# Kernel tuning notes

Measured on AMD Instinct MI355X. Metric: run time of the kernel, lower is better.

Reference implementation:

```python
import jax, jax.numpy as jnp
import numpy as np

SCALE = 8.0  # sqrt(d_k), d_k = 64

def setup_inputs() -> dict:
    key = jax.random.key(0)
    kq, kk, kv = jax.random.split(key, 3)
    B, S, D = 32, 2048, 64
    q = jax.random.normal(kq, (B, S, D), dtype=jnp.float32)
    k = jax.random.normal(kk, (B, S, D), dtype=jnp.float32)
    v = jax.random.normal(kv, (B, S, D), dtype=jnp.float32)
    return {"q": q, "k": k, "v": v}

def reference(q, k, v):
    # scores: [B, Sq, Skv]
    scores = jnp.einsum('bqd,bkd->bqk', q, k) / SCALE
    attn = jax.nn.softmax(scores, axis=2)
    # out: [B, Sq, D]
    return jnp.einsum('bqk,bkd->bqd', attn, v)
```

## Files before the change

### kernel.cpp

```cpp
#include <hip/hip_runtime.h>

#define S_N 2048
#define D_H 64
#define KVB 64
#define NT (S_N / KVB)

typedef _Float16 half8 __attribute__((ext_vector_type(8)));
typedef float floatx4 __attribute__((ext_vector_type(4)));
typedef float floatx16 __attribute__((ext_vector_type(16)));
typedef unsigned int uint2v __attribute__((ext_vector_type(2)));

__device__ __forceinline__ unsigned pkh(float a, float b) {
  return __builtin_bit_cast(unsigned, __builtin_amdgcn_cvt_pkrtz(a, b));
}
__device__ __forceinline__ float bcf(unsigned u) { return __builtin_bit_cast(float, u); }
__device__ __forceinline__ unsigned bcu(float f) { return __builtin_bit_cast(unsigned, f); }

__device__ __forceinline__ int sig(int r) { return ((r & 7) + ((r >> 3) & 7)) & 7; }

__global__ __launch_bounds__(256, 2) void sdpa_kernel(
    const float* __restrict__ Q, const float* __restrict__ K,
    const float* __restrict__ V, float* __restrict__ O) {
  const int tid = threadIdx.x;
  const int wv = tid >> 6;
  const int l = tid & 63;
  const int c31 = l & 31;
  const int hi = l >> 5;

  __shared__ _Float16 KS[2][KVB * D_H];
  __shared__ _Float16 VS[2][D_H * KVB];

  const size_t bbase = (size_t)blockIdx.y * S_N * D_H;
  const int qbase = blockIdx.x * 128 + wv * 32;
  const int qrow = qbase + c31;

  const float SCL = 0.125f * 1.44269504088896f;

  half8 qf[4];
#pragma unroll
  for (int kc = 0; kc < 4; ++kc) {
    const float* qp = Q + bbase + (size_t)qrow * D_H + kc * 16 + hi * 8;
    floatx4 x = *(const floatx4*)qp;
    floatx4 y = *(const floatx4*)(qp + 4);
    union { unsigned u[4]; half8 h; } uu = {{
        pkh(x[0] * SCL, x[1] * SCL), pkh(x[2] * SCL, x[3] * SCL),
        pkh(y[0] * SCL, y[1] * SCL), pkh(y[2] * SCL, y[3] * SCL)}};
    qf[kc] = uu.h;
  }

  const int kr_ = tid >> 3;
  const int kg8 = tid & 7;

  floatx4 kreg[2][2], vreg[2][2];

  auto loadKV = [&](int kv0) {
#pragma unroll
    for (int it = 0; it < 2; ++it) {
      const float* kp = K + bbase + (size_t)(kv0 + it * 32 + kr_) * D_H + kg8 * 8;
      kreg[it][0] = *(const floatx4*)kp;
      kreg[it][1] = *(const floatx4*)(kp + 4);
    }
#pragma unroll
    for (int r = 0; r < 2; ++r) {
      const float* vp = V + bbase + (size_t)(kv0 + 2 * kr_ + r) * D_H + kg8 * 8;
      vreg[r][0] = *(const floatx4*)vp;
      vreg[r][1] = *(const floatx4*)(vp + 4);
    }
  };

  auto writeKV = [&](int buf) {
#pragma unroll
    for (int it = 0; it < 2; ++it) {
      int row = it * 32 + kr_;
      int g = kg8 ^ sig(row);
      union { unsigned u[4]; half8 h; } uu = {{
          pkh(kreg[it][0][0], kreg[it][0][1]), pkh(kreg[it][0][2], kreg[it][0][3]),
          pkh(kreg[it][1][0], kreg[it][1][1]), pkh(kreg[it][1][2], kreg[it][1][3])}};
      *(half8*)(&KS[buf][row * 64 + g * 8]) = uu.h;
    }
#pragma unroll
    for (int jj = 0; jj < 8; ++jj) {
      int d = kg8 * 8 + jj;
      int g = (kr_ >> 2) ^ ((jj + kg8) & 7);
      unsigned val = pkh(vreg[0][jj >> 2][jj & 3], vreg[1][jj >> 2][jj & 3]);
      *(unsigned*)((char*)&VS[buf][0] + d * 128 + g * 16 + (kr_ & 3) * 4) = val;
    }
  };

  floatx16 oo[2] = {{0,0,0,0,0,0,0,0,0,0,0,0,0,0,0,0},
                    {0,0,0,0,0,0,0,0,0,0,0,0,0,0,0,0}};
  float m_ = -__builtin_inff();
  float l_ = 0.0f;

  loadKV(0);
  writeKV(0);
  __syncthreads();

  for (int t = 0; t < NT; ++t) {
    const int cur = t & 1;
    const bool pf = (t + 1) < NT;
    if (pf) loadKV((t + 1) * KVB);

    floatx16 st0 = {0,0,0,0,0,0,0,0,0,0,0,0,0,0,0,0};
    floatx16 st1 = {0,0,0,0,0,0,0,0,0,0,0,0,0,0,0,0};
    {
      const int sg0 = sig(c31), sg1 = sig(32 + c31);
#pragma unroll
      for (int kc = 0; kc < 4; ++kc) {
        half8 kf0 = *(const half8*)(&KS[cur][c31 * 64 + (((2 * kc + hi) ^ sg0) * 8)]);
        st0 = __builtin_amdgcn_mfma_f32_32x32x16_f16(kf0, qf[kc], st0, 0, 0, 0);
        half8 kf1 = *(const half8*)(&KS[cur][(32 + c31) * 64 + (((2 * kc + hi) ^ sg1) * 8)]);
        st1 = __builtin_amdgcn_mfma_f32_32x32x16_f16(kf1, qf[kc], st1, 0, 0, 0);
      }
    }

    float tm = st0[0];
#pragma unroll
    for (int r = 1; r < 16; ++r) tm = fmaxf(tm, st0[r]);
#pragma unroll
    for (int r = 0; r < 16; ++r) tm = fmaxf(tm, st1[r]);
    {
      uint2v rr = __builtin_amdgcn_permlane32_swap(bcu(tm), bcu(tm), false, false);
      tm = fmaxf(bcf(rr[0]), bcf(rr[1]));
    }
    bool skip = __all(tm <= m_ + 8.0f);
    float mn = skip ? m_ : fmaxf(m_, tm);
    float alpha = skip ? 1.0f : __builtin_amdgcn_exp2f(m_ - mn);
    m_ = mn;
    float ps = 0.0f;
#pragma unroll
    for (int r = 0; r < 16; ++r) { float p = __builtin_amdgcn_exp2f(st0[r] - mn); st0[r] = p; ps += p; }
#pragma unroll
    for (int r = 0; r < 16; ++r) { float p = __builtin_amdgcn_exp2f(st1[r] - mn); st1[r] = p; ps += p; }
    {
      uint2v rr = __builtin_amdgcn_permlane32_swap(bcu(ps), bcu(ps), false, false);
      ps = bcf(rr[0]) + bcf(rr[1]);
    }
    if (!skip) {
      l_ *= alpha;
#pragma unroll
      for (int r = 0; r < 16; ++r) { oo[0][r] *= alpha; oo[1][r] *= alpha; }
    }
    l_ += ps;

    unsigned wds[16];
#pragma unroll
    for (int j = 0; j < 8; ++j) wds[j] = pkh(st0[2 * j], st0[2 * j + 1]);
#pragma unroll
    for (int j = 0; j < 8; ++j) wds[8 + j] = pkh(st1[2 * j], st1[2 * j + 1]);
    half8 pfrag[4];
#pragma unroll
    for (int kcc = 0; kcc < 4; ++kcc) {
      int base = (kcc >> 1) * 8 + 4 * (kcc & 1);
      uint2v r0 = __builtin_amdgcn_permlane32_swap(wds[base + 0], wds[base + 2], false, false);
      uint2v r1 = __builtin_amdgcn_permlane32_swap(wds[base + 1], wds[base + 3], false, false);
      union { unsigned u[4]; half8 h; } uu = {{r0[0], r1[0], r0[1], r1[1]}};
      pfrag[kcc] = uu.h;
    }

    if (pf) writeKV(cur ^ 1);

#pragma unroll
    for (int dsub = 0; dsub < 2; ++dsub) {
      const int row = dsub * 32 + c31;
      const int sg = sig(row);
#pragma unroll
      for (int kcc = 0; kcc < 4; ++kcc) {
        half8 vf = *(const half8*)(&VS[cur][row * 64 + (((2 * kcc + hi) ^ sg) * 8)]);
        oo[dsub] = __builtin_amdgcn_mfma_f32_32x32x16_f16(vf, pfrag[kcc], oo[dsub], 0, 0, 0);
      }
    }

    __syncthreads();
  }

  float inv = 1.0f / l_;
  float* op = O + bbase + (size_t)qrow * D_H;
#pragma unroll
  for (int dsub = 0; dsub < 2; ++dsub) {
#pragma unroll
    for (int u = 0; u < 4; ++u) {
      floatx4 w;
#pragma unroll
      for (int i = 0; i < 4; ++i) w[i] = oo[dsub][4 * u + i] * inv;
      *(floatx4*)(op + dsub * 32 + u * 8 + hi * 4) = w;
    }
  }
}

extern "C" void kernel_launch(void* const* d_in, const int* in_sizes, int n_in,
                              void* d_out, int out_size, void* d_ws, size_t ws_size,
                              hipStream_t stream) {
  const float* q = (const float*)d_in[0];
  const float* k = (const float*)d_in[1];
  const float* v = (const float*)d_in[2];
  float* o = (float*)d_out;
  dim3 grid(S_N / 128, 32);
  sdpa_kernel<<<grid, dim3(256), 0, stream>>>(q, k, v, o);
}
```

Measured before the change: 145.8 us.

## Use 64-query blocks of two waves, XCD-aware block remap, tree reductions

Shrinks each workgroup from four waves (128 query rows) to two waves (64 rows), doubling the grid to 1024 blocks, and remaps the linear block id so that consecutive blocks of the same batch land on the same XCD for L2 reuse of K/V. The K/V staging loops are widened so 128 threads still fill the 64x64 tiles. Row max and sum reductions are rebalanced into trees to shorten the dependency chains. The trade-off is that each block loads K/V for fewer queries, which doubles total global K/V traffic, and with two blocks per CU there may be fewer resident waves.

```diff
diff --git a/kernel.cpp b/kernel.cpp
--- a/kernel.cpp
+++ b/kernel.cpp
@@ -4,6 +4,8 @@
 #define D_H 64
 #define KVB 64
 #define NT (S_N / KVB)
+#define QBLK 64
+#define NBLK (32 * (S_N / QBLK))
 
 typedef _Float16 half8 __attribute__((ext_vector_type(8)));
 typedef float floatx4 __attribute__((ext_vector_type(4)));
@@ -18,7 +20,7 @@
 
 __device__ __forceinline__ int sig(int r) { return ((r & 7) + ((r >> 3) & 7)) & 7; }
 
-__global__ __launch_bounds__(256, 2) void sdpa_kernel(
+__global__ __launch_bounds__(128, 2) void sdpa_kernel(
     const float* __restrict__ Q, const float* __restrict__ K,
     const float* __restrict__ V, float* __restrict__ O) {
   const int tid = threadIdx.x;
@@ -30,9 +32,13 @@
   __shared__ _Float16 KS[2][KVB * D_H];
   __shared__ _Float16 VS[2][D_H * KVB];
 
-  const size_t bbase = (size_t)blockIdx.y * S_N * D_H;
-  const int qbase = blockIdx.x * 128 + wv * 32;
-  const int qrow = qbase + c31;
+  const int bid = blockIdx.x;
+  const int nid = (bid & 7) * (NBLK / 8) + (bid >> 3);
+  const int b = nid >> 5;
+  const int qt = nid & 31;
+
+  const size_t bbase = (size_t)b * S_N * D_H;
+  const int qrow = qt * QBLK + wv * 32 + c31;
 
   const float SCL = 0.125f * 1.44269504088896f;
 
@@ -48,42 +54,51 @@
     qf[kc] = uu.h;
   }
 
-  const int kr_ = tid >> 3;
-  const int kg8 = tid & 7;
-
-  floatx4 kreg[2][2], vreg[2][2];
+  const int r8 = tid >> 3;
+  const int g8 = tid & 7;
+
+  floatx4 kreg[4][2];
+  floatx4 vreg[2][2][2];
 
   auto loadKV = [&](int kv0) {
 #pragma unroll
-    for (int it = 0; it < 2; ++it) {
-      const float* kp = K + bbase + (size_t)(kv0 + it * 32 + kr_) * D_H + kg8 * 8;
+    for (int it = 0; it < 4; ++it) {
+      const float* kp = K + bbase + (size_t)(kv0 + it * 16 + r8) * D_H + g8 * 8;
       kreg[it][0] = *(const floatx4*)kp;
       kreg[it][1] = *(const floatx4*)(kp + 4);
     }
 #pragma unroll
-    for (int r = 0; r < 2; ++r) {
-      const float* vp = V + bbase + (size_t)(kv0 + 2 * kr_ + r) * D_H + kg8 * 8;
-      vreg[r][0] = *(const floatx4*)vp;
-      vreg[r][1] = *(const floatx4*)(vp + 4);
+    for (int rr = 0; rr < 2; ++rr) {
+      int kvp = rr * 16 + r8;
+#pragma unroll
+      for (int r = 0; r < 2; ++r) {
+        const float* vp = V + bbase + (size_t)(kv0 + 2 * kvp + r) * D_H + g8 * 8;
+        vreg[rr][r][0] = *(const floatx4*)vp;
+        vreg[rr][r][1] = *(const floatx4*)(vp + 4);
+      }
     }
   };
 
   auto writeKV = [&](int buf) {
 #pragma unroll
-    for (int it = 0; it < 2; ++it) {
-      int row = it * 32 + kr_;
-      int g = kg8 ^ sig(row);
+    for (int it = 0; it < 4; ++it) {
+      int row = it * 16 + r8;
+      int g = g8 ^ sig(row);
       union { unsigned u[4]; half8 h; } uu = {{
           pkh(kreg[it][0][0], kreg[it][0][1]), pkh(kreg[it][0][2], kreg[it][0][3]),
           pkh(kreg[it][1][0], kreg[it][1][1]), pkh(kreg[it][1][2], kreg[it][1][3])}};
       *(half8*)(&KS[buf][row * 64 + g * 8]) = uu.h;
     }
 #pragma unroll
-    for (int jj = 0; jj < 8; ++jj) {
-      int d = kg8 * 8 + jj;
-      int g = (kr_ >> 2) ^ ((jj + kg8) & 7);
-      unsigned val = pkh(vreg[0][jj >> 2][jj & 3], vreg[1][jj >> 2][jj & 3]);
-      *(unsigned*)((char*)&VS[buf][0] + d * 128 + g * 16 + (kr_ & 3) * 4) = val;
+    for (int rr = 0; rr < 2; ++rr) {
+      int kvp = rr * 16 + r8;
+#pragma unroll
+      for (int jj = 0; jj < 8; ++jj) {
+        int d = g8 * 8 + jj;
+        int g = (kvp >> 2) ^ ((jj + g8) & 7);
+        unsigned val = pkh(vreg[rr][0][jj >> 2][jj & 3], vreg[rr][1][jj >> 2][jj & 3]);
+        *(unsigned*)((char*)&VS[buf][0] + d * 128 + g * 16 + (kvp & 3) * 4) = val;
+      }
     }
   };
 
@@ -114,11 +129,13 @@
       }
     }
 
-    float tm = st0[0];
-#pragma unroll
-    for (int r = 1; r < 16; ++r) tm = fmaxf(tm, st0[r]);
-#pragma unroll
-    for (int r = 0; r < 16; ++r) tm = fmaxf(tm, st1[r]);
+    float mx[8];
+#pragma unroll
+    for (int j = 0; j < 8; ++j)
+      mx[j] = fmaxf(fmaxf(st0[j], st0[j + 8]), fmaxf(st1[j], st1[j + 8]));
+    float m01 = fmaxf(mx[0], mx[1]), m23 = fmaxf(mx[2], mx[3]);
+    float m45 = fmaxf(mx[4], mx[5]), m67 = fmaxf(mx[6], mx[7]);
+    float tm = fmaxf(fmaxf(m01, m23), fmaxf(m45, m67));
     {
       uint2v rr = __builtin_amdgcn_permlane32_swap(bcu(tm), bcu(tm), false, false);
       tm = fmaxf(bcf(rr[0]), bcf(rr[1]));
@@ -127,11 +144,17 @@
     float mn = skip ? m_ : fmaxf(m_, tm);
     float alpha = skip ? 1.0f : __builtin_amdgcn_exp2f(m_ - mn);
     m_ = mn;
-    float ps = 0.0f;
-#pragma unroll
-    for (int r = 0; r < 16; ++r) { float p = __builtin_amdgcn_exp2f(st0[r] - mn); st0[r] = p; ps += p; }
-#pragma unroll
-    for (int r = 0; r < 16; ++r) { float p = __builtin_amdgcn_exp2f(st1[r] - mn); st1[r] = p; ps += p; }
+#pragma unroll
+    for (int r = 0; r < 16; ++r) st0[r] = __builtin_amdgcn_exp2f(st0[r] - mn);
+#pragma unroll
+    for (int r = 0; r < 16; ++r) st1[r] = __builtin_amdgcn_exp2f(st1[r] - mn);
+    float sp[8];
+#pragma unroll
+    for (int j = 0; j < 8; ++j)
+      sp[j] = (st0[j] + st0[j + 8]) + (st1[j] + st1[j + 8]);
+    float s01 = sp[0] + sp[1], s23 = sp[2] + sp[3];
+    float s45 = sp[4] + sp[5], s67 = sp[6] + sp[7];
+    float ps = (s01 + s23) + (s45 + s67);
     {
       uint2v rr = __builtin_amdgcn_permlane32_swap(bcu(ps), bcu(ps), false, false);
       ps = bcf(rr[0]) + bcf(rr[1]);
@@ -195,6 +218,5 @@
   const float* k = (const float*)d_in[1];
   const float* v = (const float*)d_in[2];
   float* o = (float*)d_out;
-  dim3 grid(S_N / 128, 32);
-  sdpa_kernel<<<grid, dim3(256), 0, stream>>>(q, k, v, o);
+  sdpa_kernel<<<dim3(NBLK), dim3(128), 0, stream>>>(q, k, v, o);
 }
```

New measurement: 166.9 us. +14.4%, slower.

## Quad-buffer K/V in LDS, move barrier, add MFMA priority and XCD block swizzle

Applied to the files above, without the earlier changes.

Expands the K/V LDS ring from 2 to 4 buffers so the single barrier can sit between the prefetch write and the PV MFMAs instead of at the end of each iteration. Raises wave priority around the MFMA sections and reorders the max and sum reductions into trees to shorten dependency chains. Switches to a 1D grid with a block-id swizzle that groups blocks of the same batch onto the same XCD for better L2 reuse. LDS use doubles to 64KB per block, which may limit occupancy to two blocks per CU.

```diff
diff --git a/kernel.cpp b/kernel.cpp
--- a/kernel.cpp
+++ b/kernel.cpp
@@ -4,6 +4,8 @@
 #define D_H 64
 #define KVB 64
 #define NT (S_N / KVB)
+#define QBLK 128
+#define NBLK (32 * (S_N / QBLK))
 
 typedef _Float16 half8 __attribute__((ext_vector_type(8)));
 typedef float floatx4 __attribute__((ext_vector_type(4)));
@@ -27,12 +29,16 @@
   const int c31 = l & 31;
   const int hi = l >> 5;
 
-  __shared__ _Float16 KS[2][KVB * D_H];
-  __shared__ _Float16 VS[2][D_H * KVB];
-
-  const size_t bbase = (size_t)blockIdx.y * S_N * D_H;
-  const int qbase = blockIdx.x * 128 + wv * 32;
-  const int qrow = qbase + c31;
+  __shared__ _Float16 KS[4][KVB * D_H];
+  __shared__ _Float16 VS[4][D_H * KVB];
+
+  const int bid = blockIdx.x;
+  const int nid = (bid & 7) * (NBLK / 8) + (bid >> 3);
+  const int b = nid >> 4;
+  const int qt = nid & 15;
+
+  const size_t bbase = (size_t)b * S_N * D_H;
+  const int qrow = qt * QBLK + wv * 32 + c31;
 
   const float SCL = 0.125f * 1.44269504088896f;
 
@@ -97,7 +103,7 @@
   __syncthreads();
 
   for (int t = 0; t < NT; ++t) {
-    const int cur = t & 1;
+    const int cur = t & 3;
     const bool pf = (t + 1) < NT;
     if (pf) loadKV((t + 1) * KVB);
 
@@ -105,6 +111,7 @@
     floatx16 st1 = {0,0,0,0,0,0,0,0,0,0,0,0,0,0,0,0};
     {
       const int sg0 = sig(c31), sg1 = sig(32 + c31);
+      __builtin_amdgcn_s_setprio(1);
 #pragma unroll
       for (int kc = 0; kc < 4; ++kc) {
         half8 kf0 = *(const half8*)(&KS[cur][c31 * 64 + (((2 * kc + hi) ^ sg0) * 8)]);
@@ -112,13 +119,16 @@
         half8 kf1 = *(const half8*)(&KS[cur][(32 + c31) * 64 + (((2 * kc + hi) ^ sg1) * 8)]);
         st1 = __builtin_amdgcn_mfma_f32_32x32x16_f16(kf1, qf[kc], st1, 0, 0, 0);
       }
-    }
-
-    float tm = st0[0];
-#pragma unroll
-    for (int r = 1; r < 16; ++r) tm = fmaxf(tm, st0[r]);
-#pragma unroll
-    for (int r = 0; r < 16; ++r) tm = fmaxf(tm, st1[r]);
+      __builtin_amdgcn_s_setprio(0);
+    }
+
+    float mx[8];
+#pragma unroll
+    for (int j = 0; j < 8; ++j)
+      mx[j] = fmaxf(fmaxf(st0[j], st0[j + 8]), fmaxf(st1[j], st1[j + 8]));
+    float m01 = fmaxf(mx[0], mx[1]), m23 = fmaxf(mx[2], mx[3]);
+    float m45 = fmaxf(mx[4], mx[5]), m67 = fmaxf(mx[6], mx[7]);
+    float tm = fmaxf(fmaxf(m01, m23), fmaxf(m45, m67));
     {
       uint2v rr = __builtin_amdgcn_permlane32_swap(bcu(tm), bcu(tm), false, false);
       tm = fmaxf(bcf(rr[0]), bcf(rr[1]));
@@ -127,11 +137,17 @@
     float mn = skip ? m_ : fmaxf(m_, tm);
     float alpha = skip ? 1.0f : __builtin_amdgcn_exp2f(m_ - mn);
     m_ = mn;
-    float ps = 0.0f;
-#pragma unroll
-    for (int r = 0; r < 16; ++r) { float p = __builtin_amdgcn_exp2f(st0[r] - mn); st0[r] = p; ps += p; }
-#pragma unroll
-    for (int r = 0; r < 16; ++r) { float p = __builtin_amdgcn_exp2f(st1[r] - mn); st1[r] = p; ps += p; }
+#pragma unroll
+    for (int r = 0; r < 16; ++r) st0[r] = __builtin_amdgcn_exp2f(st0[r] - mn);
+#pragma unroll
+    for (int r = 0; r < 16; ++r) st1[r] = __builtin_amdgcn_exp2f(st1[r] - mn);
+    float sp[8];
+#pragma unroll
+    for (int j = 0; j < 8; ++j)
+      sp[j] = (st0[j] + st0[j + 8]) + (st1[j] + st1[j + 8]);
+    float s01 = sp[0] + sp[1], s23 = sp[2] + sp[3];
+    float s45 = sp[4] + sp[5], s67 = sp[6] + sp[7];
+    float ps = (s01 + s23) + (s45 + s67);
     {
       uint2v rr = __builtin_amdgcn_permlane32_swap(bcu(ps), bcu(ps), false, false);
       ps = bcf(rr[0]) + bcf(rr[1]);
@@ -158,8 +174,10 @@
       pfrag[kcc] = uu.h;
     }
 
-    if (pf) writeKV(cur ^ 1);
-
+    if (pf) writeKV((t + 1) & 3);
+    __syncthreads();
+
+    __builtin_amdgcn_s_setprio(1);
 #pragma unroll
     for (int dsub = 0; dsub < 2; ++dsub) {
       const int row = dsub * 32 + c31;
@@ -170,8 +188,7 @@
         oo[dsub] = __builtin_amdgcn_mfma_f32_32x32x16_f16(vf, pfrag[kcc], oo[dsub], 0, 0, 0);
       }
     }
-
-    __syncthreads();
+    __builtin_amdgcn_s_setprio(0);
   }
 
   float inv = 1.0f / l_;
@@ -195,6 +212,5 @@
   const float* k = (const float*)d_in[1];
   const float* v = (const float*)d_in[2];
   float* o = (float*)d_out;
-  dim3 grid(S_N / 128, 32);
-  sdpa_kernel<<<grid, dim3(256), 0, stream>>>(q, k, v, o);
+  sdpa_kernel<<<dim3(NBLK), dim3(256), 0, stream>>>(q, k, v, o);
 }
```

New measurement: 137.3 us. 5.9% less time.
